# Performance work log

Hardware: AMD Instinct MI355X
Metric: run time of the kernel (lower is better)

## Reference

```python
import jax, jax.numpy as jnp
import numpy as np

K = 3
PAD = 1


def bilinear_gather(xr, py, px):
    # xr: [B, G, H, W, C] channels-last per offset group; py/px: [B, G, H, W] sample coords
    B, G, H, W, C = xr.shape
    y0 = jnp.floor(py)
    x0 = jnp.floor(px)
    wy = py - y0
    wx = px - x0
    y0i = y0.astype(jnp.int32)
    x0i = x0.astype(jnp.int32)
    bi = jnp.arange(B)[:, None, None, None]
    gi = jnp.arange(G)[None, :, None, None]
    out = jnp.zeros(py.shape + (C,), xr.dtype)
    corners = (
        (0, 0, (1 - wy) * (1 - wx)),
        (0, 1, (1 - wy) * wx),
        (1, 0, wy * (1 - wx)),
        (1, 1, wy * wx),
    )
    for dy_, dx_, w in corners:
        yy = y0i + dy_
        xx = x0i + dx_
        valid = ((yy >= 0) & (yy < H) & (xx >= 0) & (xx < W)).astype(xr.dtype)
        yc = jnp.clip(yy, 0, H - 1)
        xc = jnp.clip(xx, 0, W - 1)
        v = xr[bi, gi, yc, xc]  # [B,G,H,W,C]
        out = out + (w * valid)[..., None] * v
    return out


def setup_inputs() -> dict:
    key = jax.random.key(0)
    k1, k2, k3, k4, k5 = jax.random.split(key, 5)
    B, Cin, H, W = 4, 64, 256, 256
    G, OC = 8, 64
    KK = K * K
    x = jax.random.normal(k1, (B, Cin, H, W), jnp.float32)
    offset = jax.random.normal(k2, (B, 2, G * KK, H, W), jnp.float32)
    mask = jax.random.normal(k3, (B, G * KK, H, W), jnp.float32)
    weight = jax.random.normal(k4, (OC, Cin // G, K, K), jnp.float32) * 0.05
    bias = jax.random.normal(k5, (OC,), jnp.float32) * 0.01
    return {"x": x, "offset": offset, "mask": mask, "weight": weight, "bias": bias}


def reference(x, offset, mask, weight, bias):
    B, Cin, H, W = x.shape
    OC, Cpg, _, _ = weight.shape
    G = Cin // Cpg          # conv groups == offset groups here
    OPG = OC // G
    KK = K * K
    # replicate module's permute(0,2,1,3,4).flip(1).view(b,-1,fh,fw):
    # pair axis (dy,dx) is input dim 1; combined (group,tap) axis is reversed
    off = jnp.flip(offset, axis=2)                      # [B,2,G*KK,H,W]
    dy = off[:, 0].reshape(B, G, KK, H, W)
    dx = off[:, 1].reshape(B, G, KK, H, W)
    m = jax.nn.sigmoid(mask).reshape(B, G, KK, H, W)
    xr = x.reshape(B, G, Cpg, H, W).transpose(0, 1, 3, 4, 2)  # [B,G,H,W,Cpg]
    wg = weight.reshape(G, OPG, Cpg, K, K)
    iy = jnp.arange(H, dtype=x.dtype)[None, None, :, None]
    ix = jnp.arange(W, dtype=x.dtype)[None, None, None, :]
    out = jnp.zeros((B, G, OPG, H, W), x.dtype)
    for t in range(KK):  # fixed small loop over kernel taps
        ki, kj = t // K, t % K
        py = iy - PAD + ki + dy[:, :, t]
        px = ix - PAD + kj + dx[:, :, t]
        s = bilinear_gather(xr, py, px) * m[:, :, t][..., None]  # [B,G,H,W,Cpg]
        out = out + jnp.einsum('bghwc,gdc->bgdhw', s, wg[:, :, :, ki, kj])
    return out.reshape(B, OC, H, W) + bias[None, :, None, None]
```

## Files before the change

### kernel.cpp

```cpp
#include <hip/hip_runtime.h>
#include <hip/hip_fp16.h>


#define KSZ 3
#define PAD 1

static constexpr int B   = 4;
static constexpr int Cin = 64;
static constexpr int H   = 256;
static constexpr int W   = 256;
static constexpr int G   = 8;
static constexpr int OC  = 64;
static constexpr int KK  = KSZ * KSZ;
static constexpr int Cpg = Cin / G;
static constexpr int OPG = OC / G;
static constexpr int HW  = H * W;
static constexpr int NXCD = 8;

static constexpr int WROWS = 12;
static constexpr int WUP   = 5;
static constexpr int WPITCH = 257;

typedef _Float16 f16x8  __attribute__((ext_vector_type(8)));
typedef float    f32x16 __attribute__((ext_vector_type(16)));

union U4H {
    uint4 u;
    __half2 h2[4];
    _Float16 h[8];
    f16x8 v;
};

__global__ __launch_bounds__(256) void transpose_kernel(
    const float* __restrict__ x, uint4* __restrict__ xt)
{
    const int h = blockIdx.x, g = blockIdx.y, b = blockIdx.z;
    const int w = threadIdx.x;
    const int pix = h * W + w;
    const float* src = x + (size_t)(b * Cin + g * Cpg) * HW + pix;
    U4H v;
#pragma unroll
    for (int c = 0; c < 8; ++c) v.h[c] = (_Float16)src[(size_t)c * HW];
    xt[(size_t)(b * G + g) * HW + pix] = v.u;
}

__global__ __launch_bounds__(256, 3) void dcn_kernel(
    const uint4* __restrict__ xt,
    const float* __restrict__ offset,
    const float* __restrict__ mask,
    const float* __restrict__ weight,
    const float* __restrict__ bias,
    float* __restrict__ out)
{
    __shared__ uint4 win[WROWS * WPITCH];

    const unsigned id = blockIdx.x;
    const unsigned wl = (id & (NXCD - 1)) * (gridDim.x / NXCD) + (id >> 3);
    const int h  = wl & (H - 1);
    const int bg = wl >> 8;
    const int g  = bg & (G - 1);
    const int b  = bg >> 3;

    const int tid  = threadIdx.x;
    const int lane = tid & 63;
    const int wave = tid >> 6;
    const int hi   = lane >> 5;
    const int lp   = lane & 31;

    const uint4* xb = xt + (size_t)(b * G + g) * HW;
    const int h0 = h - WUP;

#pragma unroll
    for (int i = 0; i < WROWS; ++i) {
        const int wr = min(max(h0 + i, 0), H - 1);
        win[i * WPITCH + tid] = xb[wr * W + tid];
    }

    f16x8 afrag[5];
#pragma unroll
    for (int m = 0; m < 5; ++m) {
        f16x8 a = {};
        const int t = 2 * m + hi;
        if (lp < OPG && t < KK) {
            const float* wp = weight + (size_t)(g * OPG + lp) * Cpg * KK + t;
#pragma unroll
            for (int c = 0; c < 8; ++c) a[c] = (_Float16)wp[c * KK];
        }
        afrag[m] = a;
    }

    const float* offy = offset + (size_t)(b * 2 + 0) * (G * KK) * HW;
    const float* offx = offset + (size_t)(b * 2 + 1) * (G * KK) * HW;
    const float* mk   = mask + (size_t)b * (G * KK) * HW;

    float dyv[2][5], dxv[2][5], mvv[2][5];
#pragma unroll
    for (int tile = 0; tile < 2; ++tile) {
        const int wq  = wave * 64 + tile * 32 + lp;
        const int pix = h * W + wq;
#pragma unroll
        for (int m = 0; m < 5; ++m) {
            const int t  = 2 * m + hi;
            const int tt = (t > 8) ? 8 : t;
            const int idx0 = G * KK - 1 - (g * KK + tt);
            dyv[tile][m] = offy[(size_t)idx0 * HW + pix];
            dxv[tile][m] = offx[(size_t)idx0 * HW + pix];
            mvv[tile][m] = mk[(size_t)(g * KK + tt) * HW + pix];
        }
    }

    __syncthreads();

    auto sample = [&](int t, int wq, float dy, float dx, float mv) -> f16x8 {
        const int tt = (t > 8) ? 8 : t;
        const int ki = (tt >= 3) + (tt >= 6);
        const int kj = tt - 3 * ki;
        float msig = 1.0f / (1.0f + __expf(-mv));
        msig = (t <= 8) ? msig : 0.0f;

        const float py = (float)(h - PAD + ki) + dy;
        const float px = (float)(wq - PAD + kj) + dx;
        const float y0f = floorf(py), x0f = floorf(px);
        const float wy = py - y0f, wx = px - x0f;
        const int y0 = (int)y0f, x0 = (int)x0f;
        const int y1 = y0 + 1,   x1 = x0 + 1;
        const bool vy0 = (y0 >= 0) & (y0 < H), vy1 = (y1 >= 0) & (y1 < H);
        const bool vx0 = (x0 >= 0) & (x0 < W), vx1 = (x1 >= 0) & (x1 < W);
        const int yc0 = min(max(y0, 0), H - 1), yc1 = min(max(y1, 0), H - 1);
        const int xc0 = min(max(x0, 0), W - 1), xc1 = min(max(x1, 0), W - 1);

        float w00 = (vy0 & vx0) ? (1.f - wy) * (1.f - wx) * msig : 0.f;
        float w01 = (vy0 & vx1) ? (1.f - wy) * wx * msig : 0.f;
        float w10 = (vy1 & vx0) ? wy * (1.f - wx) * msig : 0.f;
        float w11 = (vy1 & vx1) ? wy * wx * msig : 0.f;

        const int iy0 = yc0 - h0, iy1 = yc1 - h0;
        const int i0 = min(max(iy0, 0), WROWS - 1);
        const int i1 = min(max(iy1, 0), WROWS - 1);

        uint4 v00 = win[i0 * WPITCH + xc0];
        uint4 v01 = win[i0 * WPITCH + xc1];
        uint4 v10 = win[i1 * WPITCH + xc0];
        uint4 v11 = win[i1 * WPITCH + xc1];

        const bool bad = ((unsigned)iy0 > (unsigned)(WROWS - 1)) |
                         ((unsigned)iy1 > (unsigned)(WROWS - 1));
        if (__builtin_expect(__any((int)bad), 0)) {
            if (bad) {
                v00 = xb[yc0 * W + xc0];
                v01 = xb[yc0 * W + xc1];
                v10 = xb[yc1 * W + xc0];
                v11 = xb[yc1 * W + xc1];
            }
        }

        U4H a, bq, c, d; a.u = v00; bq.u = v01; c.u = v10; d.u = v11;
        const __half2 hw00 = __float2half2_rn(w00);
        const __half2 hw01 = __float2half2_rn(w01);
        const __half2 hw10 = __float2half2_rn(w10);
        const __half2 hw11 = __float2half2_rn(w11);
        U4H s;
#pragma unroll
        for (int i = 0; i < 4; ++i)
            s.h2[i] = __hfma2(hw00, a.h2[i],
                      __hfma2(hw01, bq.h2[i],
                      __hfma2(hw10, c.h2[i],
                      __hmul2(hw11, d.h2[i]))));
        return s.v;
    };

    f32x16 acc0 = {};
    f32x16 acc1 = {};
    {
        const int wq = wave * 64 + lp;
#pragma unroll
        for (int m = 0; m < 5; ++m)
            acc0 = __builtin_amdgcn_mfma_f32_32x32x16_f16(
                afrag[m], sample(2 * m + hi, wq, dyv[0][m], dxv[0][m], mvv[0][m]), acc0, 0, 0, 0);
    }
    {
        const int wq = wave * 64 + 32 + lp;
#pragma unroll
        for (int m = 0; m < 5; ++m)
            acc1 = __builtin_amdgcn_mfma_f32_32x32x16_f16(
                afrag[m], sample(2 * m + hi, wq, dyv[1][m], dxv[1][m], mvv[1][m]), acc1, 0, 0, 0);
    }

#pragma unroll
    for (int tile = 0; tile < 2; ++tile) {
        const int wq = wave * 64 + tile * 32 + lp;
#pragma unroll
        for (int r = 0; r < 4; ++r) {
            const int dd = r + 4 * hi;
            const float v = (tile == 0 ? acc0[r] : acc1[r]) + bias[g * OPG + dd];
            out[((size_t)b * OC + g * OPG + dd) * HW + h * W + wq] = v;
        }
    }
}

extern "C" void kernel_launch(void* const* d_in, const int* in_sizes, int n_in,
                              void* d_out, int out_size, void* d_ws, size_t ws_size,
                              hipStream_t stream) {
    const float* x      = (const float*)d_in[0];
    const float* offset = (const float*)d_in[1];
    const float* mask   = (const float*)d_in[2];
    const float* weight = (const float*)d_in[3];
    const float* bias   = (const float*)d_in[4];
    float* out = (float*)d_out;
    uint4* xt  = (uint4*)d_ws;

    dim3 tgrid(H, G, B);
    dim3 block(W);
    transpose_kernel<<<tgrid, block, 0, stream>>>(x, xt);
    dcn_kernel<<<dim3(B * G * H), block, 0, stream>>>(xt, offset, mask, weight, bias, out);
}
```

Measured before the change: 114.2 us.

## Process two output rows per block sharing one shared-memory input window

Each 512-thread block now computes two adjacent output rows and loads a single 13-row LDS window for both, instead of a 12-row window per row. This cuts redundant global-to-LDS window loads by roughly half. The sigmoid of the mask is hoisted out of the sampling lambda, and the bilinear weights are factored into row and column terms. The fallback check now skips rows that are invalid anyway. Larger blocks and the 512,6 launch bound raise register pressure and may change occupancy.

```diff
diff --git a/kernel.cpp b/kernel.cpp
--- a/kernel.cpp
+++ b/kernel.cpp
@@ -17,8 +17,8 @@
 static constexpr int HW  = H * W;
 static constexpr int NXCD = 8;
 
-static constexpr int WROWS = 12;
-static constexpr int WUP   = 5;
+static constexpr int WROWS  = 13;
+static constexpr int WUP    = 5;
 static constexpr int WPITCH = 257;
 
 typedef _Float16 f16x8  __attribute__((ext_vector_type(8)));
@@ -44,7 +44,7 @@
     xt[(size_t)(b * G + g) * HW + pix] = v.u;
 }
 
-__global__ __launch_bounds__(256, 3) void dcn_kernel(
+__global__ __launch_bounds__(512, 6) void dcn_kernel(
     const uint4* __restrict__ xt,
     const float* __restrict__ offset,
     const float* __restrict__ mask,
@@ -56,24 +56,34 @@
 
     const unsigned id = blockIdx.x;
     const unsigned wl = (id & (NXCD - 1)) * (gridDim.x / NXCD) + (id >> 3);
-    const int h  = wl & (H - 1);
-    const int bg = wl >> 8;
+    const int p  = wl & (H / 2 - 1);
+    const int bg = wl >> 7;
     const int g  = bg & (G - 1);
     const int b  = bg >> 3;
+    const int h_base = 2 * p;
 
     const int tid  = threadIdx.x;
     const int lane = tid & 63;
     const int wave = tid >> 6;
+    const int row_sel = wave >> 2;
+    const int wv   = wave & 3;
     const int hi   = lane >> 5;
     const int lp   = lane & 31;
 
+    const int h  = h_base + row_sel;
+    const int h0 = h_base - WUP;
+
     const uint4* xb = xt + (size_t)(b * G + g) * HW;
-    const int h0 = h - WUP;
-
-#pragma unroll
-    for (int i = 0; i < WROWS; ++i) {
-        const int wr = min(max(h0 + i, 0), H - 1);
-        win[i * WPITCH + tid] = xb[wr * W + tid];
+
+#pragma unroll
+    for (int it = 0; it < 7; ++it) {
+        const int k = it * 512 + tid;
+        if (k < WROWS * 256) {
+            const int i   = k >> 8;
+            const int col = k & 255;
+            const int wr  = min(max(h0 + i, 0), H - 1);
+            win[i * WPITCH + col] = xb[wr * W + col];
+        }
     }
 
     f16x8 afrag[5];
@@ -93,10 +103,10 @@
     const float* offx = offset + (size_t)(b * 2 + 1) * (G * KK) * HW;
     const float* mk   = mask + (size_t)b * (G * KK) * HW;
 
-    float dyv[2][5], dxv[2][5], mvv[2][5];
+    float dyv[2][5], dxv[2][5], msv[2][5];
 #pragma unroll
     for (int tile = 0; tile < 2; ++tile) {
-        const int wq  = wave * 64 + tile * 32 + lp;
+        const int wq  = wv * 64 + tile * 32 + lp;
         const int pix = h * W + wq;
 #pragma unroll
         for (int m = 0; m < 5; ++m) {
@@ -105,48 +115,50 @@
             const int idx0 = G * KK - 1 - (g * KK + tt);
             dyv[tile][m] = offy[(size_t)idx0 * HW + pix];
             dxv[tile][m] = offx[(size_t)idx0 * HW + pix];
-            mvv[tile][m] = mk[(size_t)(g * KK + tt) * HW + pix];
+            const float mv = mk[(size_t)(g * KK + tt) * HW + pix];
+            float s = 1.0f / (1.0f + __expf(-mv));
+            msv[tile][m] = (t <= 8) ? s : 0.0f;
         }
     }
 
     __syncthreads();
 
-    auto sample = [&](int t, int wq, float dy, float dx, float mv) -> f16x8 {
+    auto sample = [&](int t, int wq, float dy, float dx, float msig) -> f16x8 {
         const int tt = (t > 8) ? 8 : t;
         const int ki = (tt >= 3) + (tt >= 6);
         const int kj = tt - 3 * ki;
-        float msig = 1.0f / (1.0f + __expf(-mv));
-        msig = (t <= 8) ? msig : 0.0f;
 
         const float py = (float)(h - PAD + ki) + dy;
         const float px = (float)(wq - PAD + kj) + dx;
         const float y0f = floorf(py), x0f = floorf(px);
         const float wy = py - y0f, wx = px - x0f;
         const int y0 = (int)y0f, x0 = (int)x0f;
-        const int y1 = y0 + 1,   x1 = x0 + 1;
-        const bool vy0 = (y0 >= 0) & (y0 < H), vy1 = (y1 >= 0) & (y1 < H);
-        const bool vx0 = (x0 >= 0) & (x0 < W), vx1 = (x1 >= 0) & (x1 < W);
-        const int yc0 = min(max(y0, 0), H - 1), yc1 = min(max(y1, 0), H - 1);
-        const int xc0 = min(max(x0, 0), W - 1), xc1 = min(max(x1, 0), W - 1);
-
-        float w00 = (vy0 & vx0) ? (1.f - wy) * (1.f - wx) * msig : 0.f;
-        float w01 = (vy0 & vx1) ? (1.f - wy) * wx * msig : 0.f;
-        float w10 = (vy1 & vx0) ? wy * (1.f - wx) * msig : 0.f;
-        float w11 = (vy1 & vx1) ? wy * wx * msig : 0.f;
-
-        const int iy0 = yc0 - h0, iy1 = yc1 - h0;
+        const bool vy0 = (y0 >= 0) & (y0 < H), vy1 = (y0 + 1 >= 0) & (y0 + 1 < H);
+        const bool vx0 = (x0 >= 0) & (x0 < W), vx1 = (x0 + 1 >= 0) & (x0 + 1 < W);
+
+        const float u   = vy0 ? (1.f - wy) * msig : 0.f;
+        const float v   = vy1 ? wy * msig : 0.f;
+        const float cx0 = vx0 ? (1.f - wx) : 0.f;
+        const float cx1 = vx1 ? wx : 0.f;
+
+        const int iy0 = y0 - h0;
+        const int iy1 = iy0 + 1;
         const int i0 = min(max(iy0, 0), WROWS - 1);
         const int i1 = min(max(iy1, 0), WROWS - 1);
+        const int xc0 = min(max(x0, 0), W - 1);
+        const int xc1 = min(max(x0 + 1, 0), W - 1);
 
         uint4 v00 = win[i0 * WPITCH + xc0];
         uint4 v01 = win[i0 * WPITCH + xc1];
         uint4 v10 = win[i1 * WPITCH + xc0];
         uint4 v11 = win[i1 * WPITCH + xc1];
 
-        const bool bad = ((unsigned)iy0 > (unsigned)(WROWS - 1)) |
-                         ((unsigned)iy1 > (unsigned)(WROWS - 1));
+        const bool bad = (vy0 & ((unsigned)iy0 > (unsigned)(WROWS - 1))) |
+                         (vy1 & ((unsigned)iy1 > (unsigned)(WROWS - 1)));
         if (__builtin_expect(__any((int)bad), 0)) {
             if (bad) {
+                const int yc0 = min(max(y0, 0), H - 1);
+                const int yc1 = min(max(y0 + 1, 0), H - 1);
                 v00 = xb[yc0 * W + xc0];
                 v01 = xb[yc0 * W + xc1];
                 v10 = xb[yc1 * W + xc0];
@@ -154,6 +166,7 @@
             }
         }
 
+        const float w00 = u * cx0, w01 = u * cx1, w10 = v * cx0, w11 = v * cx1;
         U4H a, bq, c, d; a.u = v00; bq.u = v01; c.u = v10; d.u = v11;
         const __half2 hw00 = __float2half2_rn(w00);
         const __half2 hw01 = __float2half2_rn(w01);
@@ -172,23 +185,23 @@
     f32x16 acc0 = {};
     f32x16 acc1 = {};
     {
-        const int wq = wave * 64 + lp;
+        const int wq = wv * 64 + lp;
 #pragma unroll
         for (int m = 0; m < 5; ++m)
             acc0 = __builtin_amdgcn_mfma_f32_32x32x16_f16(
-                afrag[m], sample(2 * m + hi, wq, dyv[0][m], dxv[0][m], mvv[0][m]), acc0, 0, 0, 0);
+                afrag[m], sample(2 * m + hi, wq, dyv[0][m], dxv[0][m], msv[0][m]), acc0, 0, 0, 0);
     }
     {
-        const int wq = wave * 64 + 32 + lp;
+        const int wq = wv * 64 + 32 + lp;
 #pragma unroll
         for (int m = 0; m < 5; ++m)
             acc1 = __builtin_amdgcn_mfma_f32_32x32x16_f16(
-                afrag[m], sample(2 * m + hi, wq, dyv[1][m], dxv[1][m], mvv[1][m]), acc1, 0, 0, 0);
+                afrag[m], sample(2 * m + hi, wq, dyv[1][m], dxv[1][m], msv[1][m]), acc1, 0, 0, 0);
     }
 
 #pragma unroll
     for (int tile = 0; tile < 2; ++tile) {
-        const int wq = wave * 64 + tile * 32 + lp;
+        const int wq = wv * 64 + tile * 32 + lp;
 #pragma unroll
         for (int r = 0; r < 4; ++r) {
             const int dd = r + 4 * hi;
@@ -210,7 +223,6 @@
     uint4* xt  = (uint4*)d_ws;
 
     dim3 tgrid(H, G, B);
-    dim3 block(W);
-    transpose_kernel<<<tgrid, block, 0, stream>>>(x, xt);
-    dcn_kernel<<<dim3(B * G * H), block, 0, stream>>>(xt, offset, mask, weight, bias, out);
+    transpose_kernel<<<tgrid, dim3(256), 0, stream>>>(x, xt);
+    dcn_kernel<<<dim3(B * G * H / 2), dim3(512), 0, stream>>>(xt, offset, mask, weight, bias, out);
 }
```

Result: slower. 263.7 us (+131.0%).
